# Kernel optimization log

Measured on AMD Instinct MI355X. Metric: run time of the kernel, lower is better.

The kernel has to match this reference:

```python
import jax, jax.numpy as jnp
import numpy as np
import math

EMB = 1024
HEADS = 16
VOCAB = 32000


def gelu_tanh(x):
    c = math.sqrt(2.0 / math.pi)
    return 0.5 * x * (1.0 + jnp.tanh(c * (x + 0.044715 * x * x * x)))


def layernorm(x, w, b, eps=1e-5):
    mean = jnp.mean(x, axis=-1, keepdims=True)
    var = jnp.var(x, axis=-1, keepdims=True)  # unbiased=False
    return w * ((x - mean) / jnp.sqrt(var + eps)) + b


def setup_inputs() -> dict:
    key = jax.random.key(0)
    ks = jax.random.split(key, 12)
    E, H, V = EMB, HEADS, VOCAB
    s = 1.0 / math.sqrt(E)
    return {
        "x": jax.random.normal(ks[0], (2, 2048, E), dtype=jnp.float32),
        "W_q": jax.random.normal(ks[1], (E, E), dtype=jnp.float32) * s,
        "W_k": jax.random.normal(ks[2], (E, E), dtype=jnp.float32) * s,
        "W_v": jax.random.normal(ks[3], (E, E), dtype=jnp.float32) * s,
        "ln1_w": jnp.ones((E,), jnp.float32),
        "ln1_b": jnp.zeros((E,), jnp.float32),
        "ln2_w": jnp.ones((E,), jnp.float32),
        "ln2_b": jnp.zeros((E,), jnp.float32),
        "ff_w1": jax.random.normal(ks[4], (E, 4 * E), dtype=jnp.float32) * s,
        "ff_b1": jnp.zeros((4 * E,), jnp.float32),
        "ff_w2": jax.random.normal(ks[5], (4 * E, E), dtype=jnp.float32) * (0.5 * s),
        "ff_b2": jnp.zeros((E,), jnp.float32),
        "proj_w": jax.random.normal(ks[6], (E, V), dtype=jnp.float32) * s,
        "proj_b": jnp.zeros((V,), jnp.float32),
    }


def attention(x, W_q, W_k, W_v):
    B, S, E = x.shape
    H = HEADS
    D = E // H
    q = (x @ W_q).reshape(B, S, H, D).transpose(0, 2, 1, 3)  # [B,H,S,D]
    k = (x @ W_k).reshape(B, S, H, D).transpose(0, 2, 1, 3)
    v = (x @ W_v).reshape(B, S, H, D).transpose(0, 2, 1, 3)
    scores = jnp.einsum("bhqd,bhkd->bhqk", q, k) / math.sqrt(D)
    causal = jnp.tril(jnp.ones((S, S), dtype=bool))
    scores = jnp.where(causal[None, None], scores, -jnp.inf)
    w = jax.nn.softmax(scores, axis=-1)
    ctx = jnp.einsum("bhqk,bhkd->bhqd", w, v)
    return ctx.transpose(0, 2, 1, 3).reshape(B, S, E)


def reference(x, W_q, W_k, W_v, ln1_w, ln1_b, ln2_w, ln2_b,
              ff_w1, ff_b1, ff_w2, ff_b2, proj_w, proj_b):
    # pre-LN attention block (dropout = identity, drop_rate=0)
    h = x + attention(layernorm(x, ln1_w, ln1_b), W_q, W_k, W_v)
    # pre-LN FFN block
    ff_in = layernorm(h, ln2_w, ln2_b)
    ff = gelu_tanh(ff_in @ ff_w1 + ff_b1) @ ff_w2 + ff_b2
    h = h + ff
    return h @ proj_w + proj_b
```

## Files before the change

kernel.cpp:

```cpp
#include <hip/hip_runtime.h>

using u16 = unsigned short;
typedef __attribute__((ext_vector_type(8))) short bf16x8;
typedef __attribute__((ext_vector_type(4))) float f32x4;

#define DEVI __device__ __forceinline__

DEVI float bf2f(u16 u){ union{ unsigned v; float f; } x; x.v = ((unsigned)u)<<16; return x.f; }
DEVI u16 f2bf(float f){ union{ float f; unsigned v; } x; x.f = f;
  unsigned r = x.v + 0x7FFFu + ((x.v>>16)&1u); return (u16)(r>>16); }

DEVI float gelu_f(float x){
  float y = 0.7978845608028654f*(x + 0.044715f*x*x*x);
  y = fminf(fmaxf(y, -30.f), 30.f);
  float e = __expf(2.f*y);
  return 0.5f*x*(1.f + (e-1.f)/(e+1.f));
}

DEVI void gload_lds16(const void* g, void* l){
  __builtin_amdgcn_global_load_lds((const __attribute__((address_space(1))) void*)g,
                                   (__attribute__((address_space(3))) void*)l, 16, 0, 0);
}

#define BARM asm volatile("s_barrier" ::: "memory")
#define LGKM0 asm volatile("s_waitcnt lgkmcnt(0)" ::: "memory")
#define VM8  asm volatile("s_waitcnt vmcnt(8)"  ::: "memory")
#define VM0  asm volatile("s_waitcnt vmcnt(0)"  ::: "memory")

__global__ __launch_bounds__(256) void wconv_kernel(const float* __restrict__ in,
                                                    u16* __restrict__ out, int R, int C){
  __shared__ u16 t[32][33];
  int c0 = blockIdx.x*32, r0 = blockIdx.y*32;
  int tc = threadIdx.x & 31, tr = threadIdx.x >> 5;
  #pragma unroll
  for (int i=0;i<4;i++){
    int r = tr + i*8;
    t[r][tc] = f2bf(in[(size_t)(r0+r)*C + (c0+tc)]);
  }
  __syncthreads();
  #pragma unroll
  for (int i=0;i<4;i++){
    int r = tr + i*8;
    out[(size_t)(c0+r)*R + (r0+tc)] = t[tc][r];
  }
}

DEVI void block_reduce2(float& s1, float& s2, int tid){
  #pragma unroll
  for (int off=1; off<64; off<<=1){ s1 += __shfl_xor(s1, off); s2 += __shfl_xor(s2, off); }
  __shared__ float red[8];
  int wid = tid>>6;
  if ((tid&63)==0){ red[wid*2]=s1; red[wid*2+1]=s2; }
  __syncthreads();
  s1 = red[0]+red[2]+red[4]+red[6];
  s2 = red[1]+red[3]+red[5]+red[7];
}

__global__ __launch_bounds__(256) void ln_kernel(const float* __restrict__ x,
    const float* __restrict__ w, const float* __restrict__ b, u16* __restrict__ out){
  int row = blockIdx.x, tid = threadIdx.x;
  float4 v = ((const float4*)(x + (size_t)row*1024))[tid];
  float s1 = v.x+v.y+v.z+v.w;
  float s2 = v.x*v.x+v.y*v.y+v.z*v.z+v.w*v.w;
  block_reduce2(s1,s2,tid);
  float mean = s1*(1.f/1024.f);
  float var  = s2*(1.f/1024.f) - mean*mean;
  float inv  = rsqrtf(var + 1e-5f);
  float4 wv = ((const float4*)w)[tid];
  float4 bv = ((const float4*)b)[tid];
  ushort4 o;
  o.x = f2bf(wv.x*((v.x-mean)*inv)+bv.x);
  o.y = f2bf(wv.y*((v.y-mean)*inv)+bv.y);
  o.z = f2bf(wv.z*((v.z-mean)*inv)+bv.z);
  o.w = f2bf(wv.w*((v.w-mean)*inv)+bv.w);
  ((ushort4*)(out + (size_t)row*1024))[tid] = o;
}

__global__ __launch_bounds__(256) void resln_kernel(const float* __restrict__ x,
    const u16* __restrict__ ctx, const float* __restrict__ w, const float* __restrict__ b,
    float* __restrict__ h, u16* __restrict__ hb){
  int row = blockIdx.x, tid = threadIdx.x;
  float4 xv = ((const float4*)(x + (size_t)row*1024))[tid];
  ushort4 cv = ((const ushort4*)(ctx + (size_t)row*1024))[tid];
  float4 hv;
  hv.x = xv.x + bf2f(cv.x); hv.y = xv.y + bf2f(cv.y);
  hv.z = xv.z + bf2f(cv.z); hv.w = xv.w + bf2f(cv.w);
  ((float4*)(h + (size_t)row*1024))[tid] = hv;
  float s1 = hv.x+hv.y+hv.z+hv.w;
  float s2 = hv.x*hv.x+hv.y*hv.y+hv.z*hv.z+hv.w*hv.w;
  block_reduce2(s1,s2,tid);
  float mean = s1*(1.f/1024.f);
  float var  = s2*(1.f/1024.f) - mean*mean;
  float inv  = rsqrtf(var + 1e-5f);
  float4 wv = ((const float4*)w)[tid];
  float4 bv = ((const float4*)b)[tid];
  ushort4 o;
  o.x = f2bf(wv.x*((hv.x-mean)*inv)+bv.x);
  o.y = f2bf(wv.y*((hv.y-mean)*inv)+bv.y);
  o.z = f2bf(wv.z*((hv.z-mean)*inv)+bv.z);
  o.w = f2bf(wv.w*((hv.w-mean)*inv)+bv.w);
  ((ushort4*)(hb + (size_t)row*1024))[tid] = o;
}

template<class EpiF>
DEVI void gemm8_core(const u16* __restrict__ A, const u16* __restrict__ Bt,
                     int K, int m0, int n0, EpiF epi){
  __shared__ __align__(16) u16 As[2][16384];
  __shared__ __align__(16) u16 Bs[2][16384];
  const int tid = threadIdx.x;
  const int wid = tid>>6, lane = tid&63;
  const int wr = wid>>2, wc = wid&3;
  const int g = lane>>4, l16 = lane&15;
  const int wq = wid&3;
  const int lr = lane>>3, ls = lane&7;

  f32x4 acc[8][4] = {};

  const u16* aSrc[2][2]; unsigned aDst[2][2];
  #pragma unroll
  for (int qm=0;qm<2;qm++)
    #pragma unroll
    for (int j=0;j<2;j++){
      int r = wr*128 + qm*64 + wq*16 + j*8 + lr;
      aSrc[qm][j] = A + (size_t)(m0 + r)*K + ((ls ^ (r&7))*8);
      aDst[qm][j] = (unsigned)(((wr*128 + qm*64)*8 + (wq*2+j)*64)*16);
    }
  const u16* bSrc[2][2]; unsigned bDst[2][2];
  #pragma unroll
  for (int qn=0;qn<2;qn++)
    #pragma unroll
    for (int j=0;j<2;j++){
      int r = wc*64 + qn*32 + wr*16 + j*8 + lr;
      bSrc[qn][j] = Bt + (size_t)(n0 + r)*K + ((ls ^ (r&7))*8);
      bDst[qn][j] = (unsigned)(((wc*64 + qn*32)*8 + (wr*2+j)*64)*16);
    }

  auto stageAll = [&](int buf, int kc){
    char* ab = (char*)&As[buf][0];
    char* bb = (char*)&Bs[buf][0];
    #pragma unroll
    for (int j=0;j<2;j++) gload_lds16(aSrc[0][j] + kc, ab + aDst[0][j]);
    #pragma unroll
    for (int j=0;j<2;j++) gload_lds16(bSrc[0][j] + kc, bb + bDst[0][j]);
    #pragma unroll
    for (int j=0;j<2;j++) gload_lds16(bSrc[1][j] + kc, bb + bDst[1][j]);
    #pragma unroll
    for (int j=0;j<2;j++) gload_lds16(aSrc[1][j] + kc, ab + aDst[1][j]);
  };
  auto ldA = [&](int buf, int qm, bf16x8 (&a)[4][2]){
    const char* base = (const char*)&As[buf][0];
    #pragma unroll
    for (int i=0;i<4;i++){
      int r = wr*128 + qm*64 + i*16 + l16;
      #pragma unroll
      for (int kk=0;kk<2;kk++)
        a[i][kk] = *(const bf16x8*)(base + r*128 + ((kk*64 + g*16) ^ ((l16&7)<<4)));
    }
  };
  auto ldB = [&](int buf, int qn, bf16x8 (&b)[2][2]){
    const char* base = (const char*)&Bs[buf][0];
    #pragma unroll
    for (int i=0;i<2;i++){
      int r = wc*64 + qn*32 + i*16 + l16;
      #pragma unroll
      for (int kk=0;kk<2;kk++)
        b[i][kk] = *(const bf16x8*)(base + r*128 + ((kk*64 + g*16) ^ ((l16&7)<<4)));
    }
  };
  auto mm = [&](int qm, int qn, bf16x8 (&a)[4][2], bf16x8 (&b)[2][2]){
    __builtin_amdgcn_s_setprio(1);
    #pragma unroll
    for (int i=0;i<4;i++)
      #pragma unroll
      for (int n=0;n<2;n++)
        #pragma unroll
        for (int kk=0;kk<2;kk++)
          acc[qm*4+i][qn*2+n] =
            __builtin_amdgcn_mfma_f32_16x16x32_bf16(a[i][kk], b[n][kk], acc[qm*4+i][qn*2+n], 0,0,0);
    __builtin_amdgcn_s_setprio(0);
  };

  const int NT = K>>6;
  stageAll(0, 0);
  stageAll(1, 64);

  bf16x8 a[4][2], b0[2][2], b1[2][2];
  int cur = 0;
  for (int t=0; t<NT; ++t){
    if (t < NT-1) { VM8; } else { VM0; }
    BARM;
    ldA(cur,0,a); ldB(cur,0,b0); ldB(cur,1,b1);
    mm(0,0,a,b0);
    mm(0,1,a,b1);
    ldA(cur,1,a);
    LGKM0; BARM;
    if (t+2 < NT) stageAll(cur, (t+2)<<6);
    mm(1,0,a,b0);
    mm(1,1,a,b1);
    cur ^= 1;
  }
  BARM;
  epi((char*)&As[0][0], (char*)&Bs[0][0], acc);
}

template<class EpiF>
DEVI void gemm128_core(const u16* __restrict__ A, const u16* __restrict__ Bt,
                       int K, int m0, int n0, EpiF epi){
  __shared__ __align__(16) u16 As[2][8192];
  __shared__ __align__(16) u16 Bs[2][8192];
  const int tid = threadIdx.x;
  const int wid = tid>>6, lane = tid&63;
  const int wr = wid>>1, wc = wid&1;
  const int g = lane>>4, l16 = lane&15;
  const int lr = lane>>3, ls = lane&7;

  f32x4 acc[4][4] = {};

  const u16* aSrc[4]; unsigned aDst[4];
  const u16* bSrc[4];
  #pragma unroll
  for (int j=0;j<4;j++){
    int r = wid*32 + j*8 + lr;
    aSrc[j] = A  + (size_t)(m0 + r)*K + ((ls ^ lr)*8);
    bSrc[j] = Bt + (size_t)(n0 + r)*K + ((ls ^ lr)*8);
    aDst[j] = (unsigned)((wid*32 + j*8)*128);
  }

  auto stageAll = [&](int buf, int kc){
    char* ab = (char*)&As[buf][0];
    char* bb = (char*)&Bs[buf][0];
    #pragma unroll
    for (int j=0;j<4;j++) gload_lds16(aSrc[j] + kc, ab + aDst[j]);
    #pragma unroll
    for (int j=0;j<4;j++) gload_lds16(bSrc[j] + kc, bb + aDst[j]);
  };
  auto ldA = [&](int buf, bf16x8 (&a)[4][2]){
    const char* base = (const char*)&As[buf][0];
    #pragma unroll
    for (int i=0;i<4;i++){
      int r = wr*64 + i*16 + l16;
      #pragma unroll
      for (int kk=0;kk<2;kk++)
        a[i][kk] = *(const bf16x8*)(base + r*128 + ((kk*64 + g*16) ^ ((l16&7)<<4)));
    }
  };
  auto ldB = [&](int buf, bf16x8 (&b)[4][2]){
    const char* base = (const char*)&Bs[buf][0];
    #pragma unroll
    for (int i=0;i<4;i++){
      int r = wc*64 + i*16 + l16;
      #pragma unroll
      for (int kk=0;kk<2;kk++)
        b[i][kk] = *(const bf16x8*)(base + r*128 + ((kk*64 + g*16) ^ ((l16&7)<<4)));
    }
  };

  const int NT = K>>6;
  stageAll(0, 0);
  stageAll(1, 64);

  bf16x8 a[4][2], b[4][2];
  int cur = 0;
  for (int t=0; t<NT; ++t){
    if (t < NT-1) { VM8; } else { VM0; }
    BARM;
    ldA(cur, a); ldB(cur, b);
    __builtin_amdgcn_s_setprio(1);
    #pragma unroll
    for (int i=0;i<2;i++)
      #pragma unroll
      for (int n=0;n<4;n++)
        #pragma unroll
        for (int kk=0;kk<2;kk++)
          acc[i][n] = __builtin_amdgcn_mfma_f32_16x16x32_bf16(a[i][kk], b[n][kk], acc[i][n], 0,0,0);
    __builtin_amdgcn_s_setprio(0);
    LGKM0; BARM;
    if (t+2 < NT) stageAll(cur, (t+2)<<6);
    __builtin_amdgcn_s_setprio(1);
    #pragma unroll
    for (int i=2;i<4;i++)
      #pragma unroll
      for (int n=0;n<4;n++)
        #pragma unroll
        for (int kk=0;kk<2;kk++)
          acc[i][n] = __builtin_amdgcn_mfma_f32_16x16x32_bf16(a[i][kk], b[n][kk], acc[i][n], 0,0,0);
    __builtin_amdgcn_s_setprio(0);
    cur ^= 1;
  }
  BARM;
  epi(acc);
}

DEVI int xcd_swz(int id, int nwg){ return (id&7)*(nwg>>3) + (id>>3); }

__global__ __launch_bounds__(512,2) void proj8_kernel(const u16* __restrict__ hfb,
    const u16* __restrict__ pwt, const float* __restrict__ pb, float* __restrict__ out){
  const int xcd = blockIdx.x & 7, c = blockIdx.x >> 3;
  const int mt = 2*xcd + (c & 1);
  const int nt = c >> 1;
  const int m0 = mt*256, n0 = nt*256;
  gemm8_core(hfb, pwt, 1024, m0, n0,
    [&](char* sA, char* sB, f32x4 (&acc)[8][4]){
      const int tid = threadIdx.x;
      const int wid = tid>>6, lane = tid&63;
      const int wr = wid>>2, wc = wid&3;
      const int g = lane>>4, l16 = lane&15;
      float* ep = (float*)((wid<4 ? sA : sB) + (wid&3)*16384);
      float bb[4];
      #pragma unroll
      for (int nf=0;nf<4;nf++) bb[nf] = pb[n0 + wc*64 + nf*16 + l16];
      #pragma unroll
      for (int p=0;p<2;p++){
        #pragma unroll
        for (int mf4=0;mf4<4;mf4++){
          int mf = p*4 + mf4;
          #pragma unroll
          for (int nf=0;nf<4;nf++){
            #pragma unroll
            for (int r=0;r<4;r++)
              ep[(mf4*16 + g*4 + r)*64 + nf*16 + l16] = acc[mf][nf][r] + bb[nf];
          }
        }
        LGKM0;
        #pragma unroll
        for (int it=0;it<16;it++){
          int rl = it*4 + g;
          f32x4 v = *(const f32x4*)&ep[rl*64 + l16*4];
          int grow = m0 + wr*128 + p*64 + rl;
          __builtin_nontemporal_store(v,
            (f32x4*)&out[(size_t)grow*32000 + n0 + wc*64 + l16*4]);
        }
        LGKM0;
      }
    });
}

__global__ __launch_bounds__(512,2) void ffn1_8_kernel(const u16* __restrict__ hb,
    const u16* __restrict__ w1t, const float* __restrict__ b1, u16* __restrict__ gout){
  int swz = xcd_swz(blockIdx.x, gridDim.x);
  int mt = swz & 15, nt = swz >> 4;
  const int m0 = mt*256, n0 = nt*256;
  gemm8_core(hb, w1t, 1024, m0, n0,
    [&](char*, char*, f32x4 (&acc)[8][4]){
      const int tid = threadIdx.x;
      const int wid = tid>>6, lane = tid&63;
      const int wr = wid>>2, wc = wid&3;
      const int g = lane>>4, l16 = lane&15;
      #pragma unroll
      for (int mf=0;mf<8;mf++)
        #pragma unroll
        for (int nf=0;nf<4;nf++){
          int row = m0 + wr*128 + mf*16 + g*4;
          int col = n0 + wc*64 + nf*16 + l16;
          float bb = b1[col];
          #pragma unroll
          for (int r=0;r<4;r++)
            gout[(size_t)(row+r)*4096 + col] = f2bf(gelu_f(acc[mf][nf][r] + bb));
        }
    });
}

__global__ __launch_bounds__(512,2) void qkv8_kernel(const u16* __restrict__ xn,
    const u16* __restrict__ wqt, const u16* __restrict__ wkt, const u16* __restrict__ wvt,
    u16* __restrict__ qo, u16* __restrict__ ko, u16* __restrict__ vo){
  int swz = xcd_swz(blockIdx.x, gridDim.x);
  int mt = swz & 15, ntt = swz >> 4;
  int sel = ntt >> 2;
  const u16* Bt = (sel==0)?wqt:((sel==1)?wkt:wvt);
  u16* outp = (sel==0)?qo:((sel==1)?ko:vo);
  const int m0 = mt*256, n0 = (ntt&3)*256;
  gemm8_core(xn, Bt, 1024, m0, n0,
    [&](char*, char*, f32x4 (&acc)[8][4]){
      const int tid = threadIdx.x;
      const int wid = tid>>6, lane = tid&63;
      const int wr = wid>>2, wc = wid&3;
      const int g = lane>>4, l16 = lane&15;
      #pragma unroll
      for (int mf=0;mf<8;mf++)
        #pragma unroll
        for (int nf=0;nf<4;nf++){
          int row = m0 + wr*128 + mf*16 + g*4;
          int col = n0 + wc*64 + nf*16 + l16;
          #pragma unroll
          for (int r=0;r<4;r++)
            outp[(size_t)(row+r)*1024 + col] = f2bf(acc[mf][nf][r]);
        }
    });
}

__global__ __launch_bounds__(256,2) void ffn2_kernel(const u16* __restrict__ gin,
    const u16* __restrict__ w2t, const float* __restrict__ b2,
    const float* __restrict__ h, u16* __restrict__ hfb){
  const int xcd = blockIdx.x & 7, c = blockIdx.x >> 3;
  const int mt = 4*xcd + (c & 3);
  const int nt = c >> 2;
  const int m0 = mt*128, n0 = nt*128;
  gemm128_core(gin, w2t, 4096, m0, n0,
    [&](f32x4 (&acc)[4][4]){
      const int tid = threadIdx.x;
      const int wid = tid>>6, lane = tid&63;
      const int wr = wid>>1, wc = wid&1;
      const int g = lane>>4, l16 = lane&15;
      #pragma unroll
      for (int i=0;i<4;i++)
        #pragma unroll
        for (int nf=0;nf<4;nf++){
          int row = m0 + wr*64 + i*16 + g*4;
          int col = n0 + wc*64 + nf*16 + l16;
          float bb = b2[col];
          #pragma unroll
          for (int r=0;r<4;r++)
            hfb[(size_t)(row+r)*1024 + col] =
              f2bf(h[(size_t)(row+r)*1024 + col] + acc[i][nf][r] + bb);
        }
    });
}

__global__ __launch_bounds__(256) void attn_kernel(const u16* __restrict__ q,
    const u16* __restrict__ k, const u16* __restrict__ v, u16* __restrict__ ctx){
  __shared__ u16 Qs[64*64];
  __shared__ u16 Ks[2][64*64], Vt[2][64*64];
  __shared__ u16 Ps[4][16*64];
  const int tid = threadIdx.x, lane = tid&63, wid = tid>>6;
  const int g = lane>>4, l16 = lane&15;
  const int b = blockIdx.x>>4, hh = blockIdx.x&15;
  const int qb = blockIdx.y;
  const size_t tokbase = (size_t)b*2048;
  const int hoff = hh*64;

  #pragma unroll
  for (int j=0;j<2;j++){
    int c = j*256 + tid;
    int r = c>>3, c8 = c&7;
    uint4 val = *(const uint4*)(q + (tokbase + qb*64 + r)*1024 + hoff + c8*8);
    *(uint4*)((char*)Qs + r*128 + ((c8*16) ^ ((r&7)<<4))) = val;
  }
  uint4 kreg[2], vreg[2];
  #pragma unroll
  for (int j=0;j<2;j++){
    int c = j*256 + tid;
    int r = c>>3, c8 = c&7;
    kreg[j] = *(const uint4*)(k + (tokbase + r)*1024 + hoff + c8*8);
    vreg[j] = *(const uint4*)(v + (tokbase + r)*1024 + hoff + c8*8);
  }
  #pragma unroll
  for (int j=0;j<2;j++){
    int c = j*256 + tid;
    int r = c>>3, c8 = c&7;
    *(uint4*)((char*)&Ks[0][0] + r*128 + ((c8*16) ^ ((r&7)<<4))) = kreg[j];
    union{ uint4 u; u16 s[8]; } uu; uu.u = vreg[j];
    #pragma unroll
    for (int e=0;e<8;e++){
      int d = c8*8 + e;
      *(u16*)((char*)&Vt[0][0] + d*128 + ((r*2) ^ ((d&7)<<4))) = uu.s[e];
    }
  }
  __syncthreads();

  bf16x8 qa[2];
  const int qrow_l = wid*16 + l16;
  #pragma unroll
  for (int kk=0;kk<2;kk++)
    qa[kk] = *(const bf16x8*)((const char*)Qs + qrow_l*128 + ((kk*64 + g*16) ^ ((qrow_l&7)<<4)));

  float m_r[4], l_r[4];
  f32x4 o_acc[4] = {};
  #pragma unroll
  for (int r=0;r<4;r++){ m_r[r] = -1e30f; l_r[r] = 0.f; }

  for (int kt=0; kt<=qb; kt++){
    const int cur = kt&1, nxt = cur^1;
    if (kt < qb){
      const int kv0n = (kt+1)*64;
      #pragma unroll
      for (int j=0;j<2;j++){
        int c = j*256 + tid;
        int r = c>>3, c8 = c&7;
        kreg[j] = *(const uint4*)(k + (tokbase + kv0n + r)*1024 + hoff + c8*8);
        vreg[j] = *(const uint4*)(v + (tokbase + kv0n + r)*1024 + hoff + c8*8);
      }
    }
    const int kv0 = kt*64;
    f32x4 s[4] = {};
    #pragma unroll
    for (int c=0;c<4;c++){
      #pragma unroll
      for (int kk=0;kk<2;kk++){
        int krow = c*16 + l16;
        bf16x8 kb = *(const bf16x8*)((const char*)&Ks[cur][0] + krow*128 + ((kk*64 + g*16) ^ ((krow&7)<<4)));
        s[c] = __builtin_amdgcn_mfma_f32_16x16x32_bf16(qa[kk], kb, s[c], 0,0,0);
      }
    }
    const int qrow0 = qb*64 + wid*16 + g*4;
    float sv[4][4];
    #pragma unroll
    for (int c=0;c<4;c++){
      #pragma unroll
      for (int r=0;r<4;r++){
        float xx = s[c][r] * 0.125f;
        if (kt==qb){
          int kvabs = kv0 + c*16 + l16;
          if (kvabs > qrow0 + r) xx = -1e30f;
        }
        sv[c][r] = xx;
      }
    }
    #pragma unroll
    for (int r=0;r<4;r++){
      float rm = fmaxf(fmaxf(sv[0][r],sv[1][r]),fmaxf(sv[2][r],sv[3][r]));
      #pragma unroll
      for (int off=1; off<16; off<<=1) rm = fmaxf(rm, __shfl_xor(rm, off));
      float mn  = fmaxf(m_r[r], rm);
      float fac = __expf(m_r[r] - mn);
      float rs = 0.f;
      const int prow = g*4 + r;
      #pragma unroll
      for (int c=0;c<4;c++){
        float p = __expf(sv[c][r] - mn);
        rs += p;
        *(u16*)((char*)&Ps[wid][0] + prow*128 + (((c*16+l16)*2) ^ ((prow&7)<<4))) = f2bf(p);
      }
      #pragma unroll
      for (int off=1; off<16; off<<=1) rs += __shfl_xor(rs, off);
      m_r[r] = mn;
      l_r[r] = l_r[r]*fac + rs;
      #pragma unroll
      for (int c=0;c<4;c++) o_acc[c][r] *= fac;
    }
    bf16x8 pa[2];
    #pragma unroll
    for (int kk=0;kk<2;kk++)
      pa[kk] = *(const bf16x8*)((const char*)&Ps[wid][0] + l16*128 + ((kk*64 + g*16) ^ ((l16&7)<<4)));
    #pragma unroll
    for (int c=0;c<4;c++){
      #pragma unroll
      for (int kk=0;kk<2;kk++){
        int vrow = c*16 + l16;
        bf16x8 vb = *(const bf16x8*)((const char*)&Vt[cur][0] + vrow*128 + ((kk*64 + g*16) ^ ((vrow&7)<<4)));
        o_acc[c] = __builtin_amdgcn_mfma_f32_16x16x32_bf16(pa[kk], vb, o_acc[c], 0,0,0);
      }
    }
    if (kt < qb){
      #pragma unroll
      for (int j=0;j<2;j++){
        int c = j*256 + tid;
        int r = c>>3, c8 = c&7;
        *(uint4*)((char*)&Ks[nxt][0] + r*128 + ((c8*16) ^ ((r&7)<<4))) = kreg[j];
        union{ uint4 u; u16 s[8]; } uu; uu.u = vreg[j];
        #pragma unroll
        for (int e=0;e<8;e++){
          int d = c8*8 + e;
          *(u16*)((char*)&Vt[nxt][0] + d*128 + ((r*2) ^ ((d&7)<<4))) = uu.s[e];
        }
      }
    }
    __syncthreads();
  }
  #pragma unroll
  for (int c=0;c<4;c++){
    #pragma unroll
    for (int r=0;r<4;r++){
      float o = o_acc[c][r] / l_r[r];
      size_t tok = tokbase + qb*64 + wid*16 + g*4 + r;
      ctx[tok*1024 + hoff + c*16 + l16] = f2bf(o);
    }
  }
}

extern "C" void kernel_launch(void* const* d_in, const int* in_sizes, int n_in,
                              void* d_out, int out_size, void* d_ws, size_t ws_size,
                              hipStream_t stream){
  (void)in_sizes; (void)n_in; (void)out_size; (void)ws_size;
  const float* x    = (const float*)d_in[0];
  const float* Wq   = (const float*)d_in[1];
  const float* Wk   = (const float*)d_in[2];
  const float* Wv   = (const float*)d_in[3];
  const float* ln1w = (const float*)d_in[4];
  const float* ln1b = (const float*)d_in[5];
  const float* ln2w = (const float*)d_in[6];
  const float* ln2b = (const float*)d_in[7];
  const float* fw1  = (const float*)d_in[8];
  const float* fb1  = (const float*)d_in[9];
  const float* fw2  = (const float*)d_in[10];
  const float* fb2  = (const float*)d_in[11];
  const float* pw   = (const float*)d_in[12];
  const float* pb   = (const float*)d_in[13];

  char* ob = (char*)d_out;
  u16* wqt = (u16*)(ob + 0);
  u16* wkt = (u16*)(ob + 2097152);
  u16* wvt = (u16*)(ob + 4194304);
  u16* w1t = (u16*)(ob + 6291456);
  u16* w2t = (u16*)(ob + 14680064);
  u16* xn  = (u16*)(ob + 23068672);
  u16* qbf = (u16*)(ob + 31457280);
  u16* kbf = (u16*)(ob + 39845888);
  u16* vbf = (u16*)(ob + 48234496);
  u16* ctx = (u16*)(ob + 56623104);
  float* h = (float*)(ob + 65011712);
  u16* hb  = (u16*)(ob + 81788928);
  u16* gbuf= (u16*)(ob + 90177536);

  char* wsb = (char*)d_ws;
  u16* pwt = (u16*)(wsb + 0);
  u16* hfb = (u16*)(wsb + 65536000);

  wconv_kernel<<<dim3(32,32)  ,256,0,stream>>>(Wq , wqt, 1024, 1024);
  wconv_kernel<<<dim3(32,32)  ,256,0,stream>>>(Wk , wkt, 1024, 1024);
  wconv_kernel<<<dim3(32,32)  ,256,0,stream>>>(Wv , wvt, 1024, 1024);
  wconv_kernel<<<dim3(128,32) ,256,0,stream>>>(fw1, w1t, 1024, 4096);
  wconv_kernel<<<dim3(32,128) ,256,0,stream>>>(fw2, w2t, 4096, 1024);
  wconv_kernel<<<dim3(1000,32),256,0,stream>>>(pw , pwt, 1024, 32000);

  ln_kernel    <<<4096,256,0,stream>>>(x, ln1w, ln1b, xn);
  qkv8_kernel  <<<192,512,0,stream>>>(xn, wqt, wkt, wvt, qbf, kbf, vbf);
  attn_kernel  <<<dim3(32,32),256,0,stream>>>(qbf, kbf, vbf, ctx);
  resln_kernel <<<4096,256,0,stream>>>(x, ctx, ln2w, ln2b, h, hb);
  ffn1_8_kernel<<<256,512,0,stream>>>(hb, w1t, fb1, gbuf);
  ffn2_kernel  <<<256,256,0,stream>>>(gbuf, w2t, fb2, h, hfb);
  proj8_kernel <<<2000,512,0,stream>>>(hfb, pwt, pb, (float*)d_out);
}
```

Before: 636.2 us.

## Split-K the FFN2 GEMM into two partials with a combine kernel; reverse attention block order

The FFN2 GEMM (K=4096) is split into two K-halves that run as 512 blocks instead of 256, so more of the CUs are occupied. Each half writes fp32 partials, and a new combine kernel adds the bias and residual and converts to bf16. Separately, attention query blocks are scheduled in reverse so the heavier causal tiles start first. The cost is extra global traffic for 2x16MB of partials plus one more kernel launch.

```diff
diff --git a/kernel.cpp b/kernel.cpp
--- a/kernel.cpp
+++ b/kernel.cpp
@@ -205,7 +205,7 @@
 
 template<class EpiF>
 DEVI void gemm128_core(const u16* __restrict__ A, const u16* __restrict__ Bt,
-                       int K, int m0, int n0, EpiF epi){
+                       int Kstride, int Klen, int m0, int n0, EpiF epi){
   __shared__ __align__(16) u16 As[2][8192];
   __shared__ __align__(16) u16 Bs[2][8192];
   const int tid = threadIdx.x;
@@ -221,8 +221,8 @@
   #pragma unroll
   for (int j=0;j<4;j++){
     int r = wid*32 + j*8 + lr;
-    aSrc[j] = A  + (size_t)(m0 + r)*K + ((ls ^ lr)*8);
-    bSrc[j] = Bt + (size_t)(n0 + r)*K + ((ls ^ lr)*8);
+    aSrc[j] = A  + (size_t)(m0 + r)*Kstride + ((ls ^ lr)*8);
+    bSrc[j] = Bt + (size_t)(n0 + r)*Kstride + ((ls ^ lr)*8);
     aDst[j] = (unsigned)((wid*32 + j*8)*128);
   }
 
@@ -255,7 +255,7 @@
     }
   };
 
-  const int NT = K>>6;
+  const int NT = Klen>>6;
   stageAll(0, 0);
   stageAll(1, 64);
 
@@ -388,14 +388,16 @@
     });
 }
 
-__global__ __launch_bounds__(256,2) void ffn2_kernel(const u16* __restrict__ gin,
-    const u16* __restrict__ w2t, const float* __restrict__ b2,
-    const float* __restrict__ h, u16* __restrict__ hfb){
+__global__ __launch_bounds__(256,2) void ffn2_part_kernel(const u16* __restrict__ gin,
+    const u16* __restrict__ w2t, float* __restrict__ p0, float* __restrict__ p1){
   const int xcd = blockIdx.x & 7, c = blockIdx.x >> 3;
-  const int mt = 4*xcd + (c & 3);
-  const int nt = c >> 2;
+  const int ks = c & 1;
+  const int cc = c >> 1;
+  const int mt = 4*xcd + (cc & 3);
+  const int nt = cc >> 2;
   const int m0 = mt*128, n0 = nt*128;
-  gemm128_core(gin, w2t, 4096, m0, n0,
+  float* part = ks ? p1 : p0;
+  gemm128_core(gin + ks*2048, w2t + ks*2048, 4096, 2048, m0, n0,
     [&](f32x4 (&acc)[4][4]){
       const int tid = threadIdx.x;
       const int wid = tid>>6, lane = tid&63;
@@ -407,13 +409,27 @@
         for (int nf=0;nf<4;nf++){
           int row = m0 + wr*64 + i*16 + g*4;
           int col = n0 + wc*64 + nf*16 + l16;
-          float bb = b2[col];
           #pragma unroll
           for (int r=0;r<4;r++)
-            hfb[(size_t)(row+r)*1024 + col] =
-              f2bf(h[(size_t)(row+r)*1024 + col] + acc[i][nf][r] + bb);
+            part[(size_t)(row+r)*1024 + col] = acc[i][nf][r];
         }
     });
+}
+
+__global__ __launch_bounds__(256) void ffn2_comb_kernel(const float* __restrict__ p0,
+    const float* __restrict__ p1, const float* __restrict__ b2,
+    const float* __restrict__ h, u16* __restrict__ hfb){
+  int row = blockIdx.x, tid = threadIdx.x;
+  float4 a = ((const float4*)(p0 + (size_t)row*1024))[tid];
+  float4 b = ((const float4*)(p1 + (size_t)row*1024))[tid];
+  float4 hv = ((const float4*)(h + (size_t)row*1024))[tid];
+  float4 bv = ((const float4*)b2)[tid];
+  ushort4 o;
+  o.x = f2bf(hv.x + a.x + b.x + bv.x);
+  o.y = f2bf(hv.y + a.y + b.y + bv.y);
+  o.z = f2bf(hv.z + a.z + b.z + bv.z);
+  o.w = f2bf(hv.w + a.w + b.w + bv.w);
+  ((ushort4*)(hfb + (size_t)row*1024))[tid] = o;
 }
 
 __global__ __launch_bounds__(256) void attn_kernel(const u16* __restrict__ q,
@@ -424,7 +440,7 @@
   const int tid = threadIdx.x, lane = tid&63, wid = tid>>6;
   const int g = lane>>4, l16 = lane&15;
   const int b = blockIdx.x>>4, hh = blockIdx.x&15;
-  const int qb = blockIdx.y;
+  const int qb = 31 - blockIdx.y;
   const size_t tokbase = (size_t)b*2048;
   const int hoff = hh*64;
 
@@ -600,6 +616,8 @@
   float* h = (float*)(ob + 65011712);
   u16* hb  = (u16*)(ob + 81788928);
   u16* gbuf= (u16*)(ob + 90177536);
+  float* p0= (float*)(ob + 134217728);
+  float* p1= (float*)(ob + 150994944);
 
   char* wsb = (char*)d_ws;
   u16* pwt = (u16*)(wsb + 0);
@@ -612,11 +630,12 @@
   wconv_kernel<<<dim3(32,128) ,256,0,stream>>>(fw2, w2t, 4096, 1024);
   wconv_kernel<<<dim3(1000,32),256,0,stream>>>(pw , pwt, 1024, 32000);
 
-  ln_kernel    <<<4096,256,0,stream>>>(x, ln1w, ln1b, xn);
-  qkv8_kernel  <<<192,512,0,stream>>>(xn, wqt, wkt, wvt, qbf, kbf, vbf);
-  attn_kernel  <<<dim3(32,32),256,0,stream>>>(qbf, kbf, vbf, ctx);
-  resln_kernel <<<4096,256,0,stream>>>(x, ctx, ln2w, ln2b, h, hb);
-  ffn1_8_kernel<<<256,512,0,stream>>>(hb, w1t, fb1, gbuf);
-  ffn2_kernel  <<<256,256,0,stream>>>(gbuf, w2t, fb2, h, hfb);
-  proj8_kernel <<<2000,512,0,stream>>>(hfb, pwt, pb, (float*)d_out);
-}
+  ln_kernel      <<<4096,256,0,stream>>>(x, ln1w, ln1b, xn);
+  qkv8_kernel    <<<192,512,0,stream>>>(xn, wqt, wkt, wvt, qbf, kbf, vbf);
+  attn_kernel    <<<dim3(32,32),256,0,stream>>>(qbf, kbf, vbf, ctx);
+  resln_kernel   <<<4096,256,0,stream>>>(x, ctx, ln2w, ln2b, h, hb);
+  ffn1_8_kernel  <<<256,512,0,stream>>>(hb, w1t, fb1, gbuf);
+  ffn2_part_kernel<<<512,256,0,stream>>>(gbuf, w2t, p0, p1);
+  ffn2_comb_kernel<<<4096,256,0,stream>>>(p0, p1, fb2, h, hfb);
+  proj8_kernel   <<<2000,512,0,stream>>>(hfb, pwt, pb, (float*)d_out);
+}
```

New measurement: 601.0 us. 1.06x faster.
